# Optimization experiments

Measured on AMD Instinct MI355X. Metric: run time of the kernel, lower is better.

The kernel has to match this reference:

```python
import jax, jax.numpy as jnp
import numpy as np

B, T, DIM, HEADS, DH = 4, 2048, 1024, 16, 64
MAX_SEQ_LEN = 2048


def setup_inputs() -> dict:
    key = jax.random.key(0)
    k1, k2, k3, k4 = jax.random.split(key, 4)
    x = jax.random.normal(k1, (B, T, DIM), dtype=jnp.float32)
    W_qkv = jax.random.normal(k2, (DIM, 3 * HEADS * DH), dtype=jnp.float32) * (DIM ** -0.5)
    W_0 = jax.random.normal(k3, (HEADS * DH, DIM), dtype=jnp.float32) * ((HEADS * DH) ** -0.5)
    rel_bias = jax.random.normal(k4, (2 * MAX_SEQ_LEN - 1, HEADS), dtype=jnp.float32) * 0.02
    return {"x": x, "W_qkv": W_qkv, "W_0": W_0, "rel_bias": rel_bias}


def reference(x, W_qkv, W_0, rel_bias):
    b, t, dim = x.shape
    heads = rel_bias.shape[1]
    dh = W_qkv.shape[1] // (3 * heads)
    scale = dh ** -0.5

    qkv = x @ W_qkv  # (b, t, 3*heads*dh), feature layout is (d, k, h): d slowest, h fastest
    qkv = qkv.reshape(b, t, dh, 3, heads)
    qkv = jnp.transpose(qkv, (3, 0, 4, 1, 2))  # (3, b, h, t, d)
    q, k, v = qkv[0], qkv[1], qkv[2]

    scores = jnp.einsum('bhid,bhjd->bhij', q, k) * scale  # (b, h, t, t)

    causal = jnp.tril(jnp.ones((t, t), dtype=bool))
    scores = jnp.where(causal[None, None], scores, -jnp.inf)

    # relative position bias: index = j - i + t - 1
    rel_idx = jnp.arange(t)[None, :] - jnp.arange(t)[:, None] + (t - 1)  # (t, t)
    bias = rel_bias[rel_idx]  # (t, t, heads)
    scores = scores + jnp.transpose(bias, (2, 0, 1))[None]

    attn = jax.nn.softmax(scores, axis=-1)
    out = jnp.einsum('bhij,bhjd->bhid', attn, v)  # (b, h, t, d)
    out = jnp.transpose(out, (0, 2, 1, 3)).reshape(b, t, heads * dh)
    return out @ W_0
```

## Files before the change

### kernel.cpp

```cpp
#include <hip/hip_runtime.h>
#include <hip/hip_bf16.h>
#include <stdint.h>

#define B_ 4
#define T_ 2048
#define NH 16
#define DH 64
#define DIM 1024
#define NF 3072

typedef unsigned short u16;
typedef uint32_t u32;
typedef __bf16 bf16;
typedef bf16 bf16x8 __attribute__((ext_vector_type(8)));
typedef float f32x4 __attribute__((ext_vector_type(4)));
typedef u16 u16x8 __attribute__((ext_vector_type(8)));
typedef u16 u16x4 __attribute__((ext_vector_type(4)));

__device__ __forceinline__ u16 f2bf(float f) {
    u32 u = __builtin_bit_cast(u32, f);
    u = (u + 0x7fffu + ((u >> 16) & 1u)) >> 16;
    return (u16)u;
}

__device__ __forceinline__ float exp2f_fast(float x) {
#if __has_builtin(__builtin_amdgcn_exp2f)
    return __builtin_amdgcn_exp2f(x);
#else
    return exp2f(x);
#endif
}

#define GLOAD16(g, l)                                                          \
    __builtin_amdgcn_global_load_lds(                                          \
        (const __attribute__((address_space(1))) u32*)(g),                     \
        (__attribute__((address_space(3))) u32*)(l), 16, 0, 0)


__global__ __launch_bounds__(256) void cvt_bf16_k(const float* __restrict__ src,
                                                  u16* __restrict__ dst, int n8) {
    int i = blockIdx.x * 256 + threadIdx.x;
    if (i >= n8) return;
    const float4* s = (const float4*)src + (size_t)i * 2;
    float4 a = s[0], b = s[1];
    u16x8 o;
    o[0]=f2bf(a.x); o[1]=f2bf(a.y); o[2]=f2bf(a.z); o[3]=f2bf(a.w);
    o[4]=f2bf(b.x); o[5]=f2bf(b.y); o[6]=f2bf(b.z); o[7]=f2bf(b.w);
    *(u16x8*)(dst + (size_t)i * 8) = o;
}

template <int PERM>
__global__ __launch_bounds__(256) void wcvt_t_k(const float* __restrict__ src,
                                                u16* __restrict__ dst, int K, int N) {
    __shared__ float tile[32][33];
    int n0 = blockIdx.x * 32, k0 = blockIdx.y * 32;
    int c = threadIdx.x & 31, r0 = threadIdx.x >> 5;
#pragma unroll
    for (int i = 0; i < 4; i++) {
        int r = r0 + i * 8;
        tile[r][c] = src[(size_t)(k0 + r) * N + n0 + c];
    }
    __syncthreads();
#pragma unroll
    for (int i = 0; i < 4; i++) {
        int r = r0 + i * 8;
        int n = n0 + r;
        int nd;
        if (PERM) {
            int d = n / 48, rem = n - d * 48;
            int kk = rem >> 4, h = rem & 15;
            nd = kk * 1024 + h * 64 + d;
        } else {
            nd = n;
        }
        dst[(size_t)nd * K + k0 + c] = f2bf(tile[c][r]);
    }
}

__global__ __launch_bounds__(256) void rbt_k(const float* __restrict__ rb,
                                             u16* __restrict__ rbT2,
                                             u16* __restrict__ rbT2s) {
    int i = blockIdx.x * 256 + threadIdx.x;
    if (i >= NH * 4096) return;
    int h = i >> 12, d = i & 4095;
    float v = (d <= 2047) ? rb[(size_t)d * NH + h] * 1.44269504f : -1e30f;
    rbT2[i] = __builtin_bit_cast(u16, (bf16)v);
    int d2 = d + 1;
    float v2 = (d2 <= 2047) ? rb[(size_t)d2 * NH + h] * 1.44269504f : -1e30f;
    rbT2s[i] = __builtin_bit_cast(u16, (bf16)v2);
}

__global__ __launch_bounds__(256) void transpose_v_k(const u16* __restrict__ qkvF,
                                                     u16* __restrict__ Vt) {
    __shared__ __align__(16) u16 tile[64][72];
    int bh = blockIdx.y;
    int h = bh & 15, b = bh >> 4;
    int t0 = blockIdx.x * 64;
    const u16* src = qkvF + ((size_t)b * T_ + t0) * NF + 2048 + h * 64;
    for (int idx = threadIdx.x; idx < 512; idx += 256) {
        int r = idx >> 3, ch = idx & 7;
        *(u16x8*)&tile[r][ch * 8] = *(const u16x8*)&src[(size_t)r * NF + ch * 8];
    }
    __syncthreads();
    u16* dst = Vt + (size_t)bh * DH * T_ + t0;
    for (int idx = threadIdx.x; idx < 512; idx += 256) {
        int d = idx >> 3, ch = idx & 7;
        u16x8 v;
#pragma unroll
        for (int e = 0; e < 8; e++) v[e] = tile[ch * 8 + e][d];
        *(u16x8*)&dst[(size_t)d * T_ + ch * 8] = v;
    }
}


template <int WRITE_BF16>
__global__ __launch_bounds__(256, 2) void gemm_bt_k(const u16* __restrict__ A,
                                                    const u16* __restrict__ Bt,
                                                    void* __restrict__ Cout,
                                                    int M, int N, int K) {
    __shared__ __align__(16) u16 As[128 * 32];
    __shared__ __align__(16) u16 Bs[128 * 32];
    const int tid = threadIdx.x;
    const int wave = tid >> 6, lane = tid & 63;
    const int bm = blockIdx.x, bn = blockIdx.y;
    const int wr = (wave >> 1) * 64, wc = (wave & 1) * 64;
    const int lrow = lane & 15, lk = (lane >> 4) * 8;
    const int srow = lane >> 2;
    const int sk = (lane & 3) * 8;
    const u16* Ab = A + (size_t)(bm * 128 + wave * 32) * K;
    const u16* Bb = Bt + (size_t)(bn * 128 + wave * 32) * K;
    u16* AsW = As + wave * 1024;
    u16* BsW = Bs + wave * 1024;
    f32x4 acc[4][4] = {};

    for (int k0 = 0; k0 < K; k0 += 32) {
        __syncthreads();
        GLOAD16(Ab + (size_t)srow * K + k0 + sk, AsW);
        GLOAD16(Ab + (size_t)(srow + 16) * K + k0 + sk, AsW + 512);
        GLOAD16(Bb + (size_t)srow * K + k0 + sk, BsW);
        GLOAD16(Bb + (size_t)(srow + 16) * K + k0 + sk, BsW + 512);
        __syncthreads();
        bf16x8 af[4], bfr[4];
#pragma unroll
        for (int i = 0; i < 4; i++) af[i] = *(const bf16x8*)&As[(wr + i * 16 + lrow) * 32 + lk];
#pragma unroll
        for (int j = 0; j < 4; j++) bfr[j] = *(const bf16x8*)&Bs[(wc + j * 16 + lrow) * 32 + lk];
#pragma unroll
        for (int i = 0; i < 4; i++)
#pragma unroll
            for (int j = 0; j < 4; j++)
                acc[i][j] = __builtin_amdgcn_mfma_f32_16x16x32_bf16(af[i], bfr[j], acc[i][j], 0, 0, 0);
    }

    const int crow = (lane >> 4) * 4, ccol = lane & 15;
#pragma unroll
    for (int i = 0; i < 4; i++)
#pragma unroll
        for (int j = 0; j < 4; j++) {
            int gm = bm * 128 + wr + i * 16 + crow;
            int gn = bn * 128 + wc + j * 16 + ccol;
#pragma unroll
            for (int r = 0; r < 4; r++) {
                if (WRITE_BF16)
                    ((u16*)Cout)[(size_t)(gm + r) * N + gn] = f2bf(acc[i][j][r]);
                else
                    ((float*)Cout)[(size_t)(gm + r) * N + gn] = acc[i][j][r];
            }
        }
}

__global__ __launch_bounds__(256, 4) void flash_attn_k(const u16* __restrict__ qkvF,
                                                       const u16* __restrict__ Vt,
                                                       const u16* __restrict__ rbT2,
                                                       const u16* __restrict__ rbT2s,
                                                       u16* __restrict__ O) {
    __shared__ __align__(16) u16 Ks[64 * 64];
    __shared__ __align__(16) u16 Vs[64 * 64];
    __shared__ __align__(16) u16 Ps[4][16 * 64];
    __shared__ __align__(16) u16 rbs2a[4096];
    __shared__ __align__(16) u16 rbs2b[4096];
    const int tid = threadIdx.x, wave = tid >> 6, lane = tid & 63;
    const int Lid = blockIdx.x;
    const int c = Lid & 7, u = Lid >> 3;
    const int bh = ((u & 7) << 3) | c;
    const int pair = u >> 3;
    const int h = bh & 15, b = bh >> 4;
    const int l15 = lane & 15, g4 = lane >> 4;
    const float SC2 = 0.125f * 1.44269504f;

    {
        *(u16x8*)&rbs2a[tid * 8] = *(const u16x8*)&rbT2[(size_t)h * 4096 + tid * 8];
        *(u16x8*)&rbs2a[2048 + tid * 8] = *(const u16x8*)&rbT2[(size_t)h * 4096 + 2048 + tid * 8];
        *(u16x8*)&rbs2b[tid * 8] = *(const u16x8*)&rbT2s[(size_t)h * 4096 + tid * 8];
        *(u16x8*)&rbs2b[2048 + tid * 8] = *(const u16x8*)&rbT2s[(size_t)h * 4096 + 2048 + tid * 8];
    }

    const size_t trow = (size_t)b * T_;
    const int srow = tid >> 2;
    const int sch = tid & 3;
    u16* pw = &Ps[wave][0];
    const u16* kgb = &qkvF[(trow + srow) * NF + 1024 + h * 64];
    const u16* vgb = &Vt[((size_t)bh * DH + srow) * T_];

    u16x8 kv0 = *(const u16x8*)&kgb[sch * 8];
    u16x8 kv1 = *(const u16x8*)&kgb[(sch + 4) * 8];
    u16x8 vv0 = *(const u16x8*)&vgb[sch * 8];
    u16x8 vv1 = *(const u16x8*)&vgb[(sch + 4) * 8];

    for (int half = 0; half < 2; half++) {
        const int blk = half ? 31 - pair : pair;
        const int q0 = blk * 64 + wave * 16;
        bf16x8 aq[2];
        aq[0] = *(const bf16x8*)&qkvF[(trow + q0 + l15) * NF + h * 64 + g4 * 8];
        aq[1] = *(const bf16x8*)&qkvF[(trow + q0 + l15) * NF + h * 64 + 32 + g4 * 8];

        const int ib0 = 2047 - l15 + g4 * 4 - q0;
        const u32* b32 = (const u32*)((ib0 & 1) ? &rbs2b[ib0 - 1] : &rbs2a[ib0]);

        f32x4 oacc[4] = {};
        float l_r = 0.f;

        for (int jt = 0; jt <= blk; jt++) {
            const int j0 = jt * 64;
            __syncthreads();
            {
                int sw = srow & 7;
                *(u16x8*)&Ks[srow * 64 + ((sch ^ sw) * 8)] = kv0;
                *(u16x8*)&Ks[srow * 64 + (((sch + 4) ^ sw) * 8)] = kv1;
                *(u16x8*)&Vs[srow * 64 + ((sch ^ sw) * 8)] = vv0;
                *(u16x8*)&Vs[srow * 64 + (((sch + 4) ^ sw) * 8)] = vv1;
            }
            __syncthreads();
            {
                int njt = jt + 1;
                int j0n = (njt <= blk) ? njt * 64 : (half == 0 ? 0 : -1);
                if (j0n >= 0) {
                    const u16* kg = kgb + (size_t)j0n * NF;
                    const u16* vg = vgb + j0n;
                    kv0 = *(const u16x8*)&kg[sch * 8];
                    kv1 = *(const u16x8*)&kg[(sch + 4) * 8];
                    vv0 = *(const u16x8*)&vg[sch * 8];
                    vv1 = *(const u16x8*)&vg[(sch + 4) * 8];
                }
            }
            f32x4 s[4];
#pragma unroll
            for (int ni = 0; ni < 4; ni++) {
                f32x4 z = {};
                s[ni] = z;
            }
            __builtin_amdgcn_s_setprio(1);
#pragma unroll
            for (int ni = 0; ni < 4; ni++) {
                int arow = ni * 16 + l15;
#pragma unroll
                for (int kk = 0; kk < 2; kk++) {
                    int ch = kk * 4 + g4;
                    bf16x8 ak = *(const bf16x8*)&Ks[arow * 64 + ((ch ^ (arow & 7)) * 8)];
                    s[ni] = __builtin_amdgcn_mfma_f32_16x16x32_bf16(ak, aq[kk], s[ni], 0, 0, 0);
                }
            }
            __builtin_amdgcn_s_setprio(0);
            float p[4][4];
            float su = 0.f;
            const int jo = j0 >> 1;
#pragma unroll
            for (int ni = 0; ni < 4; ni++) {
                u32 w0 = b32[jo + ni * 8];
                u32 w1 = b32[jo + ni * 8 + 1];
                float bz[4];
                bz[0] = __builtin_bit_cast(float, w0 << 16);
                bz[1] = __builtin_bit_cast(float, w0 & 0xffff0000u);
                bz[2] = __builtin_bit_cast(float, w1 << 16);
                bz[3] = __builtin_bit_cast(float, w1 & 0xffff0000u);
#pragma unroll
                for (int r = 0; r < 4; r++) {
                    float e = exp2f_fast(fmaf(s[ni][r], SC2, bz[r]));
                    p[ni][r] = e;
                    su += e;
                }
            }
            su += __shfl_xor(su, 16);
            su += __shfl_xor(su, 32);
            l_r += su;
#pragma unroll
            for (int ni = 0; ni < 4; ni++) {
                u16x4 pk;
#pragma unroll
                for (int r = 0; r < 4; r++)
                    pk[r] = __builtin_bit_cast(u16, (bf16)p[ni][r]);
                int colb = ni * 16 + g4 * 4;
                int ch = colb >> 3, co = colb & 7;
                *(u16x4*)&pw[l15 * 64 + ((ch ^ (l15 & 7)) * 8) + co] = pk;
            }
            bf16x8 bp[2];
#pragma unroll
            for (int kk = 0; kk < 2; kk++) {
                int ch = kk * 4 + g4;
                bp[kk] = *(const bf16x8*)&pw[l15 * 64 + ((ch ^ (l15 & 7)) * 8)];
            }
            __builtin_amdgcn_s_setprio(1);
#pragma unroll
            for (int di = 0; di < 4; di++) {
                int vrow = di * 16 + l15;
#pragma unroll
                for (int kk = 0; kk < 2; kk++) {
                    int ch = kk * 4 + g4;
                    bf16x8 av = *(const bf16x8*)&Vs[vrow * 64 + ((ch ^ (vrow & 7)) * 8)];
                    oacc[di] = __builtin_amdgcn_mfma_f32_16x16x32_bf16(av, bp[kk], oacc[di], 0, 0, 0);
                }
            }
            __builtin_amdgcn_s_setprio(0);
        }
        float inv = 1.0f / l_r;
        u16* orow = &O[((size_t)b * T_ + q0 + l15) * (NH * DH) + h * DH];
#pragma unroll
        for (int di = 0; di < 4; di++) {
            u16x4 ov;
#pragma unroll
            for (int r = 0; r < 4; r++)
                ov[r] = __builtin_bit_cast(u16, (bf16)(oacc[di][r] * inv));
            *(u16x4*)&orow[di * 16 + g4 * 4] = ov;
        }
    }
}


extern "C" void kernel_launch(void* const* d_in, const int* in_sizes, int n_in,
                              void* d_out, int out_size, void* d_ws, size_t ws_size,
                              hipStream_t stream) {
    const float* x    = (const float*)d_in[0];
    const float* Wqkv = (const float*)d_in[1];
    const float* W0   = (const float*)d_in[2];
    const float* rb   = (const float*)d_in[3];
    char* ws = (char*)d_ws;

    u16*   xb    = (u16*)(ws + 0);
    u16*   WqkvT = (u16*)(ws + 16777216);
    u16*   W0T   = (u16*)(ws + 23068672);
    u16*   rbT2  = (u16*)(ws + 25165824);
    u16*   rbT2s = (u16*)(ws + 25296896);
    u16*   qkvF  = (u16*)(ws + 25559040);
    u16*   attnO = (u16*)(ws + 75890688);
    u16*   Vtb   = (u16*)(ws + 0);

    cvt_bf16_k<<<4096, 256, 0, stream>>>(x, xb, (B_ * T_ * DIM) / 8);
    wcvt_t_k<1><<<dim3(NF / 32, DIM / 32), 256, 0, stream>>>(Wqkv, WqkvT, DIM, NF);
    wcvt_t_k<0><<<dim3(DIM / 32, DIM / 32), 256, 0, stream>>>(W0, W0T, DIM, DIM);
    rbt_k<<<(NH * 4096 + 255) / 256, 256, 0, stream>>>(rb, rbT2, rbT2s);

    gemm_bt_k<1><<<dim3((B_ * T_) / 128, NF / 128), 256, 0, stream>>>(
        xb, WqkvT, qkvF, B_ * T_, NF, DIM);

    transpose_v_k<<<dim3(T_ / 64, B_ * NH), 256, 0, stream>>>(qkvF, Vtb);

    flash_attn_k<<<1024, 256, 0, stream>>>(qkvF, Vtb, rbT2, rbT2s, attnO);

    gemm_bt_k<0><<<dim3((B_ * T_) / 128, DIM / 128), 256, 0, stream>>>(
        attnO, W0T, d_out, B_ * T_, DIM, DIM);
}
```

Baseline: 189.7 us.

## Process two query tiles per wave to share K/V tile loads in attention

```diff
diff --git a/kernel.cpp b/kernel.cpp
--- a/kernel.cpp
+++ b/kernel.cpp
@@ -169,14 +169,14 @@
         }
 }
 
-__global__ __launch_bounds__(256, 4) void flash_attn_k(const u16* __restrict__ qkvF,
+__global__ __launch_bounds__(256, 2) void flash_attn_k(const u16* __restrict__ qkvF,
                                                        const u16* __restrict__ Vt,
                                                        const u16* __restrict__ rbT2,
                                                        const u16* __restrict__ rbT2s,
                                                        u16* __restrict__ O) {
     __shared__ __align__(16) u16 Ks[64 * 64];
     __shared__ __align__(16) u16 Vs[64 * 64];
-    __shared__ __align__(16) u16 Ps[4][16 * 64];
+    __shared__ __align__(16) u16 Ps[4][2][16 * 64];
     __shared__ __align__(16) u16 rbs2a[4096];
     __shared__ __align__(16) u16 rbs2b[4096];
     const int tid = threadIdx.x, wave = tid >> 6, lane = tid & 63;
@@ -198,7 +198,8 @@
     const size_t trow = (size_t)b * T_;
     const int srow = tid >> 2;
     const int sch = tid & 3;
-    u16* pw = &Ps[wave][0];
+    u16* pwA = &Ps[wave][0][0];
+    u16* pwB = &Ps[wave][1][0];
     const u16* kgb = &qkvF[(trow + srow) * NF + 1024 + h * 64];
     const u16* vgb = &Vt[((size_t)bh * DH + srow) * T_];
 
@@ -208,19 +209,24 @@
     u16x8 vv1 = *(const u16x8*)&vgb[(sch + 4) * 8];
 
     for (int half = 0; half < 2; half++) {
-        const int blk = half ? 31 - pair : pair;
-        const int q0 = blk * 64 + wave * 16;
-        bf16x8 aq[2];
-        aq[0] = *(const bf16x8*)&qkvF[(trow + q0 + l15) * NF + h * 64 + g4 * 8];
-        aq[1] = *(const bf16x8*)&qkvF[(trow + q0 + l15) * NF + h * 64 + 32 + g4 * 8];
-
-        const int ib0 = 2047 - l15 + g4 * 4 - q0;
-        const u32* b32 = (const u32*)((ib0 & 1) ? &rbs2b[ib0 - 1] : &rbs2a[ib0]);
-
-        f32x4 oacc[4] = {};
-        float l_r = 0.f;
-
-        for (int jt = 0; jt <= blk; jt++) {
+        const int blk = half ? 15 - pair : pair;
+        const int qbA = blk * 128 + wave * 16;
+        const int qbB = qbA + 64;
+        bf16x8 aqA[2], aqB[2];
+        aqA[0] = *(const bf16x8*)&qkvF[(trow + qbA + l15) * NF + h * 64 + g4 * 8];
+        aqA[1] = *(const bf16x8*)&qkvF[(trow + qbA + l15) * NF + h * 64 + 32 + g4 * 8];
+        aqB[0] = *(const bf16x8*)&qkvF[(trow + qbB + l15) * NF + h * 64 + g4 * 8];
+        aqB[1] = *(const bf16x8*)&qkvF[(trow + qbB + l15) * NF + h * 64 + 32 + g4 * 8];
+
+        const int ibA = 2047 - l15 + g4 * 4 - qbA;
+        const u32* b32A = (const u32*)((ibA & 1) ? &rbs2b[ibA - 1] : &rbs2a[ibA]);
+        const u32* b32B = b32A - 32;
+
+        f32x4 oaccA[4] = {}, oaccB[4] = {};
+        float lA = 0.f, lB = 0.f;
+
+        const int jtmax = 2 * blk + 1;
+        for (int jt = 0; jt <= jtmax; jt++) {
             const int j0 = jt * 64;
             __syncthreads();
             {
@@ -233,7 +239,7 @@
             __syncthreads();
             {
                 int njt = jt + 1;
-                int j0n = (njt <= blk) ? njt * 64 : (half == 0 ? 0 : -1);
+                int j0n = (njt <= jtmax) ? njt * 64 : (half == 0 ? 0 : -1);
                 if (j0n >= 0) {
                     const u16* kg = kgb + (size_t)j0n * NF;
                     const u16* vg = vgb + j0n;
@@ -243,11 +249,12 @@
                     vv1 = *(const u16x8*)&vg[(sch + 4) * 8];
                 }
             }
-            f32x4 s[4];
+            f32x4 sA[4], sB[4];
 #pragma unroll
             for (int ni = 0; ni < 4; ni++) {
                 f32x4 z = {};
-                s[ni] = z;
+                sA[ni] = z;
+                sB[ni] = z;
             }
             __builtin_amdgcn_s_setprio(1);
 #pragma unroll
@@ -257,47 +264,67 @@
                 for (int kk = 0; kk < 2; kk++) {
                     int ch = kk * 4 + g4;
                     bf16x8 ak = *(const bf16x8*)&Ks[arow * 64 + ((ch ^ (arow & 7)) * 8)];
-                    s[ni] = __builtin_amdgcn_mfma_f32_16x16x32_bf16(ak, aq[kk], s[ni], 0, 0, 0);
+                    sA[ni] = __builtin_amdgcn_mfma_f32_16x16x32_bf16(ak, aqA[kk], sA[ni], 0, 0, 0);
+                    sB[ni] = __builtin_amdgcn_mfma_f32_16x16x32_bf16(ak, aqB[kk], sB[ni], 0, 0, 0);
                 }
             }
             __builtin_amdgcn_s_setprio(0);
-            float p[4][4];
-            float su = 0.f;
             const int jo = j0 >> 1;
-#pragma unroll
-            for (int ni = 0; ni < 4; ni++) {
-                u32 w0 = b32[jo + ni * 8];
-                u32 w1 = b32[jo + ni * 8 + 1];
-                float bz[4];
-                bz[0] = __builtin_bit_cast(float, w0 << 16);
-                bz[1] = __builtin_bit_cast(float, w0 & 0xffff0000u);
-                bz[2] = __builtin_bit_cast(float, w1 << 16);
-                bz[3] = __builtin_bit_cast(float, w1 & 0xffff0000u);
-#pragma unroll
-                for (int r = 0; r < 4; r++) {
-                    float e = exp2f_fast(fmaf(s[ni][r], SC2, bz[r]));
-                    p[ni][r] = e;
-                    su += e;
+            {
+                float su = 0.f;
+#pragma unroll
+                for (int ni = 0; ni < 4; ni++) {
+                    u32 w0 = b32A[jo + ni * 8];
+                    u32 w1 = b32A[jo + ni * 8 + 1];
+                    float e0 = exp2f_fast(fmaf(sA[ni][0], SC2, __builtin_bit_cast(float, w0 << 16)));
+                    float e1 = exp2f_fast(fmaf(sA[ni][1], SC2, __builtin_bit_cast(float, w0 & 0xffff0000u)));
+                    float e2 = exp2f_fast(fmaf(sA[ni][2], SC2, __builtin_bit_cast(float, w1 << 16)));
+                    float e3 = exp2f_fast(fmaf(sA[ni][3], SC2, __builtin_bit_cast(float, w1 & 0xffff0000u)));
+                    su += (e0 + e1) + (e2 + e3);
+                    u16x4 pk;
+                    pk[0] = __builtin_bit_cast(u16, (bf16)e0);
+                    pk[1] = __builtin_bit_cast(u16, (bf16)e1);
+                    pk[2] = __builtin_bit_cast(u16, (bf16)e2);
+                    pk[3] = __builtin_bit_cast(u16, (bf16)e3);
+                    int colb = ni * 16 + g4 * 4;
+                    int ch = colb >> 3, co = colb & 7;
+                    *(u16x4*)&pwA[l15 * 64 + ((ch ^ (l15 & 7)) * 8) + co] = pk;
                 }
-            }
-            su += __shfl_xor(su, 16);
-            su += __shfl_xor(su, 32);
-            l_r += su;
-#pragma unroll
-            for (int ni = 0; ni < 4; ni++) {
-                u16x4 pk;
-#pragma unroll
-                for (int r = 0; r < 4; r++)
-                    pk[r] = __builtin_bit_cast(u16, (bf16)p[ni][r]);
-                int colb = ni * 16 + g4 * 4;
-                int ch = colb >> 3, co = colb & 7;
-                *(u16x4*)&pw[l15 * 64 + ((ch ^ (l15 & 7)) * 8) + co] = pk;
-            }
-            bf16x8 bp[2];
+                su += __shfl_xor(su, 16);
+                su += __shfl_xor(su, 32);
+                lA += su;
+            }
+            {
+                float su = 0.f;
+#pragma unroll
+                for (int ni = 0; ni < 4; ni++) {
+                    u32 w0 = b32B[jo + ni * 8];
+                    u32 w1 = b32B[jo + ni * 8 + 1];
+                    float e0 = exp2f_fast(fmaf(sB[ni][0], SC2, __builtin_bit_cast(float, w0 << 16)));
+                    float e1 = exp2f_fast(fmaf(sB[ni][1], SC2, __builtin_bit_cast(float, w0 & 0xffff0000u)));
+                    float e2 = exp2f_fast(fmaf(sB[ni][2], SC2, __builtin_bit_cast(float, w1 << 16)));
+                    float e3 = exp2f_fast(fmaf(sB[ni][3], SC2, __builtin_bit_cast(float, w1 & 0xffff0000u)));
+                    su += (e0 + e1) + (e2 + e3);
+                    u16x4 pk;
+                    pk[0] = __builtin_bit_cast(u16, (bf16)e0);
+                    pk[1] = __builtin_bit_cast(u16, (bf16)e1);
+                    pk[2] = __builtin_bit_cast(u16, (bf16)e2);
+                    pk[3] = __builtin_bit_cast(u16, (bf16)e3);
+                    int colb = ni * 16 + g4 * 4;
+                    int ch = colb >> 3, co = colb & 7;
+                    *(u16x4*)&pwB[l15 * 64 + ((ch ^ (l15 & 7)) * 8) + co] = pk;
+                }
+                su += __shfl_xor(su, 16);
+                su += __shfl_xor(su, 32);
+                lB += su;
+            }
+            bf16x8 bpA[2], bpB[2];
 #pragma unroll
             for (int kk = 0; kk < 2; kk++) {
                 int ch = kk * 4 + g4;
-                bp[kk] = *(const bf16x8*)&pw[l15 * 64 + ((ch ^ (l15 & 7)) * 8)];
+                int off = l15 * 64 + ((ch ^ (l15 & 7)) * 8);
+                bpA[kk] = *(const bf16x8*)&pwA[off];
+                bpB[kk] = *(const bf16x8*)&pwB[off];
             }
             __builtin_amdgcn_s_setprio(1);
 #pragma unroll
@@ -307,20 +334,35 @@
                 for (int kk = 0; kk < 2; kk++) {
                     int ch = kk * 4 + g4;
                     bf16x8 av = *(const bf16x8*)&Vs[vrow * 64 + ((ch ^ (vrow & 7)) * 8)];
-                    oacc[di] = __builtin_amdgcn_mfma_f32_16x16x32_bf16(av, bp[kk], oacc[di], 0, 0, 0);
+                    oaccA[di] = __builtin_amdgcn_mfma_f32_16x16x32_bf16(av, bpA[kk], oaccA[di], 0, 0, 0);
+                    oaccB[di] = __builtin_amdgcn_mfma_f32_16x16x32_bf16(av, bpB[kk], oaccB[di], 0, 0, 0);
                 }
             }
             __builtin_amdgcn_s_setprio(0);
         }
-        float inv = 1.0f / l_r;
-        u16* orow = &O[((size_t)b * T_ + q0 + l15) * (NH * DH) + h * DH];
-#pragma unroll
-        for (int di = 0; di < 4; di++) {
-            u16x4 ov;
-#pragma unroll
-            for (int r = 0; r < 4; r++)
-                ov[r] = __builtin_bit_cast(u16, (bf16)(oacc[di][r] * inv));
-            *(u16x4*)&orow[di * 16 + g4 * 4] = ov;
+        {
+            float inv = 1.0f / lA;
+            u16* orow = &O[((size_t)b * T_ + qbA + l15) * (NH * DH) + h * DH];
+#pragma unroll
+            for (int di = 0; di < 4; di++) {
+                u16x4 ov;
+#pragma unroll
+                for (int r = 0; r < 4; r++)
+                    ov[r] = __builtin_bit_cast(u16, (bf16)(oaccA[di][r] * inv));
+                *(u16x4*)&orow[di * 16 + g4 * 4] = ov;
+            }
+        }
+        {
+            float inv = 1.0f / lB;
+            u16* orow = &O[((size_t)b * T_ + qbB + l15) * (NH * DH) + h * DH];
+#pragma unroll
+            for (int di = 0; di < 4; di++) {
+                u16x4 ov;
+#pragma unroll
+                for (int r = 0; r < 4; r++)
+                    ov[r] = __builtin_bit_cast(u16, (bf16)(oaccB[di][r] * inv));
+                *(u16x4*)&orow[di * 16 + g4 * 4] = ov;
+            }
         }
     }
 }
@@ -354,7 +396,7 @@
 
     transpose_v_k<<<dim3(T_ / 64, B_ * NH), 256, 0, stream>>>(qkvF, Vtb);
 
-    flash_attn_k<<<1024, 256, 0, stream>>>(qkvF, Vtb, rbT2, rbT2s, attnO);
+    flash_attn_k<<<512, 256, 0, stream>>>(qkvF, Vtb, rbT2, rbT2s, attnO);
 
     gemm_bt_k<0><<<dim3((B_ * T_) / 128, DIM / 128), 256, 0, stream>>>(
         attnO, W0T, d_out, B_ * T_, DIM, DIM);
```

Measured after the change: 188.6 us. No clear change (-0.6%).
